# Kernel optimization log

Hardware: AMD Instinct MI355X
Metric: run time of the kernel (lower is better)

The kernel has to match this reference:

```python
import jax, jax.numpy as jnp
import numpy as np

N_NODES = 100000


def _sage_conv(x, src, dst, Wl, Wr, b):
    # mean aggregation of source features onto destination nodes (PyG SAGEConv default)
    msgs = x[src]                                             # [E, d] irregular gather
    agg = jax.ops.segment_sum(msgs, dst, num_segments=N_NODES)
    cnt = jax.ops.segment_sum(jnp.ones((src.shape[0], 1), x.dtype), dst,
                              num_segments=N_NODES)
    agg = agg / jnp.maximum(cnt, 1.0)                         # mean; isolated nodes -> 0
    return agg @ Wl.T + x @ Wr.T + b                          # W_l * agg + W_r * x + b


def setup_inputs() -> dict:
    key = jax.random.key(0)
    ks = jax.random.split(key, 7)
    d_in, d_hid, d_out = 64, 64, 40
    n_edges = 1200000
    x = jax.random.normal(ks[0], (N_NODES, d_in), dtype=jnp.float32)
    edge_index = jax.random.randint(ks[1], (2, n_edges), 0, N_NODES, dtype=jnp.int64)
    s1 = 1.0 / np.sqrt(d_in)
    s2 = 1.0 / np.sqrt(d_hid)
    return {
        "x": x,
        "edge_index": edge_index,
        "W1l": jax.random.normal(ks[2], (d_hid, d_in), dtype=jnp.float32) * s1,
        "W1r": jax.random.normal(ks[3], (d_hid, d_in), dtype=jnp.float32) * s1,
        "b1": jnp.zeros((d_hid,), dtype=jnp.float32),
        "W2l": jax.random.normal(ks[4], (d_out, d_hid), dtype=jnp.float32) * s2,
        "W2r": jax.random.normal(ks[5], (d_out, d_hid), dtype=jnp.float32) * s2,
        "b2": jnp.zeros((d_out,), dtype=jnp.float32),
    }


def reference(x, edge_index, W1l, W1r, b1, W2l, W2r, b2):
    src, dst = edge_index[0], edge_index[1]
    h = _sage_conv(x, src, dst, W1l, W1r, b1)
    h = jax.nn.relu(h)
    # F.dropout(p=0.5) in eval mode is identity (deterministic reference)
    out = _sage_conv(h, src, dst, W2l, W2r, b2)
    return out
```

## Files before the change

kernel.cpp:

```cpp
#include <hip/hip_runtime.h>
#include <hip/hip_bf16.h>

__device__ __forceinline__ float bf2f(unsigned short u) {
    return __uint_as_float(((unsigned int)u) << 16);
}
__device__ __forceinline__ unsigned short f2bf(float f) {
    unsigned int u = __float_as_uint(f);
    return (unsigned short)((u + 0x7FFFu + ((u >> 16) & 1u)) >> 16);
}

__device__ __forceinline__ bool is_i64(const int* __restrict__ e) {
    int z = 0;
#pragma unroll
    for (int i = 0; i < 16; ++i) z |= e[2 * i + 1];
    return z == 0;
}

template <int OUT_DIM, int GST>
__global__ __launch_bounds__(256) void gemm1_hist_fused(
        const float* __restrict__ in, const float* __restrict__ Wl,
        const float* __restrict__ Wr, const float* __restrict__ bias,
        unsigned short* __restrict__ gout, float* __restrict__ sout,
        int n_nodes, int gemmBlocks,
        const int* __restrict__ eidx, int n_edges,
        int* __restrict__ deg, int* __restrict__ rank) {
    __shared__ unsigned int sWp[64][65];
    __shared__ float sB[OUT_DIM];
    __shared__ float sX[4][8][68];

    if ((int)blockIdx.x >= gemmBlocks) {
        const int half = (n_edges + 1) / 2;
        const int e = (blockIdx.x - gemmBlocks) * blockDim.x + threadIdx.x;
        if (e >= half) return;
        const bool i64 = is_i64(eidx);
        {
            int d = i64 ? eidx[2 * (n_edges + e)] : eidx[n_edges + e];
            rank[e] = atomicAdd(&deg[d], 1);
        }
        const int e2 = e + half;
        if (e2 < n_edges) {
            int d = i64 ? eidx[2 * (n_edges + e2)] : eidx[n_edges + e2];
            rank[e2] = atomicAdd(&deg[d], 1);
        }
        return;
    }

    for (int idx = threadIdx.x; idx < OUT_DIM * 64; idx += 256) {
        const int r = idx >> 6, c = idx & 63;
        sWp[c][r] = (unsigned int)f2bf(Wl[idx]) | ((unsigned int)f2bf(Wr[idx]) << 16);
    }
    if (threadIdx.x < OUT_DIM) sB[threadIdx.x] = bias[threadIdx.x];
    __syncthreads();

    const int g = threadIdx.x >> 6;
    const int j = threadIdx.x & 63;
    const bool jv = (j < OUT_DIM);
    const int jj = jv ? j : 0;
    const int blockBase = blockIdx.x * 128;

#pragma unroll 1
    for (int it = 0; it < 4; ++it) {
        const int nb = blockBase + it * 32 + g * 8;
        if (nb >= n_nodes) break;
#pragma unroll
        for (int n = 0; n < 8; ++n) {
            const int node = nb + n;
            sX[g][n][j] = (node < n_nodes) ? in[(size_t)node * 64 + j] : 0.0f;
        }
        float al[8], ar[8];
#pragma unroll
        for (int n = 0; n < 8; ++n) { al[n] = 0.0f; ar[n] = 0.0f; }

#pragma unroll 2
        for (int q = 0; q < 16; ++q) {
            const unsigned int w0 = sWp[4 * q + 0][jj];
            const unsigned int w1 = sWp[4 * q + 1][jj];
            const unsigned int w2 = sWp[4 * q + 2][jj];
            const unsigned int w3 = sWp[4 * q + 3][jj];
            const float4 x0 = *(const float4*)&sX[g][0][4 * q];
            const float4 x1 = *(const float4*)&sX[g][1][4 * q];
            const float4 x2 = *(const float4*)&sX[g][2][4 * q];
            const float4 x3 = *(const float4*)&sX[g][3][4 * q];
            const float4 x4 = *(const float4*)&sX[g][4][4 * q];
            const float4 x5 = *(const float4*)&sX[g][5][4 * q];
            const float4 x6 = *(const float4*)&sX[g][6][4 * q];
            const float4 x7 = *(const float4*)&sX[g][7][4 * q];
#define DG_STEP(WP, M)                                                         \
            {                                                                  \
                const float wl_ = __uint_as_float((WP) << 16);                 \
                const float wr_ = __uint_as_float((WP) & 0xFFFF0000u);         \
                al[0] = fmaf(x0.M, wl_, al[0]); ar[0] = fmaf(x0.M, wr_, ar[0]);\
                al[1] = fmaf(x1.M, wl_, al[1]); ar[1] = fmaf(x1.M, wr_, ar[1]);\
                al[2] = fmaf(x2.M, wl_, al[2]); ar[2] = fmaf(x2.M, wr_, ar[2]);\
                al[3] = fmaf(x3.M, wl_, al[3]); ar[3] = fmaf(x3.M, wr_, ar[3]);\
                al[4] = fmaf(x4.M, wl_, al[4]); ar[4] = fmaf(x4.M, wr_, ar[4]);\
                al[5] = fmaf(x5.M, wl_, al[5]); ar[5] = fmaf(x5.M, wr_, ar[5]);\
                al[6] = fmaf(x6.M, wl_, al[6]); ar[6] = fmaf(x6.M, wr_, ar[6]);\
                al[7] = fmaf(x7.M, wl_, al[7]); ar[7] = fmaf(x7.M, wr_, ar[7]);\
            }
            DG_STEP(w0, x)
            DG_STEP(w1, y)
            DG_STEP(w2, z)
            DG_STEP(w3, w)
#undef DG_STEP
        }

        const float bb = jv ? sB[jj] : 0.0f;
#pragma unroll
        for (int n = 0; n < 8; ++n) {
            const int node = nb + n;
            if (node < n_nodes) {
                if (jv) {
                    gout[(size_t)node * GST + j] = f2bf(al[n]);
                    sout[(size_t)node * OUT_DIM + j] = ar[n] + bb;
                } else if (j < GST) {
                    gout[(size_t)node * GST + j] = 0;
                }
            }
        }
    }
}

__global__ void hist_rank_kernel(const int* __restrict__ eidx, int n_edges,
                                 int* __restrict__ deg, int* __restrict__ rank) {
    const int half = (n_edges + 1) / 2;
    const int e = blockIdx.x * blockDim.x + threadIdx.x;
    if (e >= half) return;
    const bool i64 = is_i64(eidx);
    {
        int d = i64 ? eidx[2 * (n_edges + e)] : eidx[n_edges + e];
        rank[e] = atomicAdd(&deg[d], 1);
    }
    const int e2 = e + half;
    if (e2 < n_edges) {
        int d = i64 ? eidx[2 * (n_edges + e2)] : eidx[n_edges + e2];
        rank[e2] = atomicAdd(&deg[d], 1);
    }
}

__global__ void fill_rank_kernel(const int* __restrict__ eidx, int n_edges,
                                 const int* __restrict__ off, const int* __restrict__ rank,
                                 int* __restrict__ csr) {
    const int half = (n_edges + 1) / 2;
    const int e = blockIdx.x * blockDim.x + threadIdx.x;
    if (e >= half) return;
    const bool i64 = is_i64(eidx);
    {
        int s, d;
        if (i64) { s = eidx[2 * e]; d = eidx[2 * (n_edges + e)]; }
        else     { s = eidx[e];     d = eidx[n_edges + e]; }
        __builtin_nontemporal_store(s, &csr[off[d] + rank[e]]);
    }
    const int e2 = e + half;
    if (e2 < n_edges) {
        int s, d;
        if (i64) { s = eidx[2 * e2]; d = eidx[2 * (n_edges + e2)]; }
        else     { s = eidx[e2];     d = eidx[n_edges + e2]; }
        __builtin_nontemporal_store(s, &csr[off[d] + rank[e2]]);
    }
}

__global__ void fill_kernel(const int* __restrict__ eidx, int n_edges,
                            int* __restrict__ cursor, int* __restrict__ csr) {
    int e = blockIdx.x * blockDim.x + threadIdx.x;
    if (e >= n_edges) return;
    const bool i64 = is_i64(eidx);
    int s, d;
    if (i64) { s = eidx[2 * e]; d = eidx[2 * (n_edges + e)]; }
    else     { s = eidx[e];     d = eidx[n_edges + e]; }
    int pos = atomicAdd(&cursor[d], 1);
    csr[pos] = s;
}

#define TILE 1024
__global__ void scan_p1(const int* __restrict__ deg, int* __restrict__ bsum, int n) {
    __shared__ int red[256];
    const int t = threadIdx.x;
    const int base = blockIdx.x * TILE + t * 4;
    int s = 0;
#pragma unroll
    for (int k = 0; k < 4; ++k) { int i = base + k; if (i < n) s += deg[i]; }
    red[t] = s;
    __syncthreads();
    for (int d = 128; d > 0; d >>= 1) {
        if (t < d) red[t] += red[t + d];
        __syncthreads();
    }
    if (t == 0) bsum[blockIdx.x] = red[0];
}

__global__ void scan_p2(int* __restrict__ bsum, int* __restrict__ off, int nb, int n) {
    __shared__ int s[1024];
    const int t = threadIdx.x;
    s[t] = (t < nb) ? bsum[t] : 0;
    __syncthreads();
    for (int d = 1; d < 1024; d <<= 1) {
        int v = (t >= d) ? s[t - d] : 0;
        __syncthreads();
        s[t] += v;
        __syncthreads();
    }
    if (t < nb) bsum[t] = (t == 0) ? 0 : s[t - 1];
    if (t == 0) off[n] = s[nb - 1];
}

__global__ void scan_p3(const int* __restrict__ deg, const int* __restrict__ bsum,
                        int* __restrict__ off, int* __restrict__ cursor, int n) {
    __shared__ int red[256];
    const int t = threadIdx.x;
    const int base = blockIdx.x * TILE + t * 4;
    int v0 = 0, v1 = 0, v2 = 0, v3 = 0;
    if (base + 0 < n) v0 = deg[base + 0];
    if (base + 1 < n) v1 = deg[base + 1];
    if (base + 2 < n) v2 = deg[base + 2];
    if (base + 3 < n) v3 = deg[base + 3];
    const int mysum = v0 + v1 + v2 + v3;
    red[t] = mysum;
    __syncthreads();
    for (int d = 1; d < 256; d <<= 1) {
        int u = (t >= d) ? red[t - d] : 0;
        __syncthreads();
        red[t] += u;
        __syncthreads();
    }
    int run = bsum[blockIdx.x] + red[t] - mysum;
    if (base + 0 < n) { off[base + 0] = run; cursor[base + 0] = run; run += v0; }
    if (base + 1 < n) { off[base + 1] = run; cursor[base + 1] = run; run += v1; }
    if (base + 2 < n) { off[base + 2] = run; cursor[base + 2] = run; run += v2; }
    if (base + 3 < n) { off[base + 3] = run; cursor[base + 3] = run; run += v3; }
}

template <int OUT_DIM, int GST>
__global__ __launch_bounds__(256) void dual_gemm3(
        const float* __restrict__ in,
        const float* __restrict__ Wl, const float* __restrict__ Wr,
        const float* __restrict__ bias,
        unsigned short* __restrict__ gout,
        float* __restrict__ sout,
        int n_nodes) {
    __shared__ unsigned int sWp[64][65];
    __shared__ float sB[OUT_DIM];
    __shared__ float sX[4][8][68];

    for (int idx = threadIdx.x; idx < OUT_DIM * 64; idx += 256) {
        const int r = idx >> 6, c = idx & 63;
        sWp[c][r] = (unsigned int)f2bf(Wl[idx]) | ((unsigned int)f2bf(Wr[idx]) << 16);
    }
    if (threadIdx.x < OUT_DIM) sB[threadIdx.x] = bias[threadIdx.x];
    __syncthreads();

    const int g = threadIdx.x >> 6;
    const int j = threadIdx.x & 63;
    const bool jv = (j < OUT_DIM);
    const int jj = jv ? j : 0;
    const int blockBase = blockIdx.x * 128;

#pragma unroll 1
    for (int it = 0; it < 4; ++it) {
        const int nb = blockBase + it * 32 + g * 8;
        if (nb >= n_nodes) break;
#pragma unroll
        for (int n = 0; n < 8; ++n) {
            const int node = nb + n;
            sX[g][n][j] = (node < n_nodes) ? in[(size_t)node * 64 + j] : 0.0f;
        }
        float al[8], ar[8];
#pragma unroll
        for (int n = 0; n < 8; ++n) { al[n] = 0.0f; ar[n] = 0.0f; }

#pragma unroll 2
        for (int q = 0; q < 16; ++q) {
            const unsigned int w0 = sWp[4 * q + 0][jj];
            const unsigned int w1 = sWp[4 * q + 1][jj];
            const unsigned int w2 = sWp[4 * q + 2][jj];
            const unsigned int w3 = sWp[4 * q + 3][jj];
            const float4 x0 = *(const float4*)&sX[g][0][4 * q];
            const float4 x1 = *(const float4*)&sX[g][1][4 * q];
            const float4 x2 = *(const float4*)&sX[g][2][4 * q];
            const float4 x3 = *(const float4*)&sX[g][3][4 * q];
            const float4 x4 = *(const float4*)&sX[g][4][4 * q];
            const float4 x5 = *(const float4*)&sX[g][5][4 * q];
            const float4 x6 = *(const float4*)&sX[g][6][4 * q];
            const float4 x7 = *(const float4*)&sX[g][7][4 * q];
#define DG_STEP(WP, M)                                                         \
            {                                                                  \
                const float wl_ = __uint_as_float((WP) << 16);                 \
                const float wr_ = __uint_as_float((WP) & 0xFFFF0000u);         \
                al[0] = fmaf(x0.M, wl_, al[0]); ar[0] = fmaf(x0.M, wr_, ar[0]);\
                al[1] = fmaf(x1.M, wl_, al[1]); ar[1] = fmaf(x1.M, wr_, ar[1]);\
                al[2] = fmaf(x2.M, wl_, al[2]); ar[2] = fmaf(x2.M, wr_, ar[2]);\
                al[3] = fmaf(x3.M, wl_, al[3]); ar[3] = fmaf(x3.M, wr_, ar[3]);\
                al[4] = fmaf(x4.M, wl_, al[4]); ar[4] = fmaf(x4.M, wr_, ar[4]);\
                al[5] = fmaf(x5.M, wl_, al[5]); ar[5] = fmaf(x5.M, wr_, ar[5]);\
                al[6] = fmaf(x6.M, wl_, al[6]); ar[6] = fmaf(x6.M, wr_, ar[6]);\
                al[7] = fmaf(x7.M, wl_, al[7]); ar[7] = fmaf(x7.M, wr_, ar[7]);\
            }
            DG_STEP(w0, x)
            DG_STEP(w1, y)
            DG_STEP(w2, z)
            DG_STEP(w3, w)
#undef DG_STEP
        }

        const float bb = jv ? sB[jj] : 0.0f;
#pragma unroll
        for (int n = 0; n < 8; ++n) {
            const int node = nb + n;
            if (node < n_nodes) {
                if (jv) {
                    gout[(size_t)node * GST + j] = f2bf(al[n]);
                    sout[(size_t)node * OUT_DIM + j] = ar[n] + bb;
                } else if (j < GST) {
                    gout[(size_t)node * GST + j] = 0;
                }
            }
        }
    }
}

template <int SRC_STRIDE, int CGROUPS, int OUT_DIM, bool RELU>
__global__ __launch_bounds__(256) void gather_addmul_bf16(
        const unsigned short* __restrict__ gsrc,
        const float* __restrict__ sadd,
        const int* __restrict__ off, const int* __restrict__ csr,
        float* __restrict__ out, int n_nodes) {
    const int l = threadIdx.x & 63;
    const int wave = (int)((blockIdx.x * blockDim.x + threadIdx.x) >> 6);
    const int c = l & 15, r = l >> 4;
    const bool cact = (c < CGROUPS);
    const int n0 = wave * 8;

    for (int n = n0; n < n0 + 8; ++n) {
        if (n >= n_nodes) return;
        const int e0 = off[n], e1 = off[n + 1];
        float4 a0 = {0.f,0.f,0.f,0.f}, a1 = a0, a2 = a0, a3 = a0;
        for (int i = e0; i < e1; i += 16) {
            const int i0 = i + r, i1 = i0 + 4, i2 = i0 + 8, i3 = i0 + 12;
            if (cact && i0 < e1) {
                const int s = csr[i0];
                const ushort4 u = *(const ushort4*)(gsrc + (size_t)s * SRC_STRIDE + 4 * c);
                a0.x += bf2f(u.x); a0.y += bf2f(u.y); a0.z += bf2f(u.z); a0.w += bf2f(u.w);
            }
            if (cact && i1 < e1) {
                const int s = csr[i1];
                const ushort4 u = *(const ushort4*)(gsrc + (size_t)s * SRC_STRIDE + 4 * c);
                a1.x += bf2f(u.x); a1.y += bf2f(u.y); a1.z += bf2f(u.z); a1.w += bf2f(u.w);
            }
            if (cact && i2 < e1) {
                const int s = csr[i2];
                const ushort4 u = *(const ushort4*)(gsrc + (size_t)s * SRC_STRIDE + 4 * c);
                a2.x += bf2f(u.x); a2.y += bf2f(u.y); a2.z += bf2f(u.z); a2.w += bf2f(u.w);
            }
            if (cact && i3 < e1) {
                const int s = csr[i3];
                const ushort4 u = *(const ushort4*)(gsrc + (size_t)s * SRC_STRIDE + 4 * c);
                a3.x += bf2f(u.x); a3.y += bf2f(u.y); a3.z += bf2f(u.z); a3.w += bf2f(u.w);
            }
        }
        float4 a;
        a.x = (a0.x + a1.x) + (a2.x + a3.x);
        a.y = (a0.y + a1.y) + (a2.y + a3.y);
        a.z = (a0.z + a1.z) + (a2.z + a3.z);
        a.w = (a0.w + a1.w) + (a2.w + a3.w);
        a.x += __shfl_xor(a.x, 16); a.y += __shfl_xor(a.y, 16);
        a.z += __shfl_xor(a.z, 16); a.w += __shfl_xor(a.w, 16);
        a.x += __shfl_xor(a.x, 32); a.y += __shfl_xor(a.y, 32);
        a.z += __shfl_xor(a.z, 32); a.w += __shfl_xor(a.w, 32);
        const int deg = e1 - e0;
        const float inv = (deg > 0) ? 1.0f / (float)deg : 0.0f;
        if (4 * l < OUT_DIM) {
            const float4 sv = *(const float4*)(sadd + (size_t)n * OUT_DIM + 4 * l);
            float4 o;
            o.x = fmaf(a.x, inv, sv.x);
            o.y = fmaf(a.y, inv, sv.y);
            o.z = fmaf(a.z, inv, sv.z);
            o.w = fmaf(a.w, inv, sv.w);
            if (RELU) {
                o.x = fmaxf(o.x, 0.f); o.y = fmaxf(o.y, 0.f);
                o.z = fmaxf(o.z, 0.f); o.w = fmaxf(o.w, 0.f);
            }
            *(float4*)(out + (size_t)n * OUT_DIM + 4 * l) = o;
        }
    }
}

#define NPB 32
template <int OUT_DIM, bool RELU>
__global__ __launch_bounds__(512, 8) void fused_layer_f4(
        const float* __restrict__ feat,
        const int* __restrict__ off, const int* __restrict__ csr,
        const float* __restrict__ Wl, const float* __restrict__ Wr,
        const float* __restrict__ bias,
        float* __restrict__ out, int n_nodes) {
    __shared__ float sWl[OUT_DIM][65];
    __shared__ float sWr[OUT_DIM][65];
    __shared__ float sB[OUT_DIM];
    __shared__ float sA[8][64];
    __shared__ float sX[8][64];

    for (int idx = threadIdx.x; idx < OUT_DIM * 64; idx += 512) {
        sWl[idx >> 6][idx & 63] = Wl[idx];
        sWr[idx >> 6][idx & 63] = Wr[idx];
    }
    if (threadIdx.x < OUT_DIM) sB[threadIdx.x] = bias[threadIdx.x];
    __syncthreads();

    const int g = threadIdx.x >> 6;
    const int l = threadIdx.x & 63;
    const int c = l & 15, r = l >> 4;
    const int base = blockIdx.x * NPB;

#pragma unroll 1
    for (int it = 0; it < NPB / 8; ++it) {
        const int node = base + it * 8 + g;
        if (node >= n_nodes) break;
        const int e0 = off[node], e1 = off[node + 1];
        const float selfv = feat[(size_t)node * 64 + l];
        float4 a0 = {0.f,0.f,0.f,0.f}, a1 = a0, a2 = a0, a3 = a0;
        for (int i = e0; i < e1; i += 16) {
            const int i0 = i + r, i1 = i0 + 4, i2 = i0 + 8, i3 = i0 + 12;
            if (i0 < e1) { const int s = csr[i0];
                const float4 v = *(const float4*)(feat + (size_t)s * 64 + 4 * c);
                a0.x += v.x; a0.y += v.y; a0.z += v.z; a0.w += v.w; }
            if (i1 < e1) { const int s = csr[i1];
                const float4 v = *(const float4*)(feat + (size_t)s * 64 + 4 * c);
                a1.x += v.x; a1.y += v.y; a1.z += v.z; a1.w += v.w; }
            if (i2 < e1) { const int s = csr[i2];
                const float4 v = *(const float4*)(feat + (size_t)s * 64 + 4 * c);
                a2.x += v.x; a2.y += v.y; a2.z += v.z; a2.w += v.w; }
            if (i3 < e1) { const int s = csr[i3];
                const float4 v = *(const float4*)(feat + (size_t)s * 64 + 4 * c);
                a3.x += v.x; a3.y += v.y; a3.z += v.z; a3.w += v.w; }
        }
        float4 a;
        a.x = (a0.x + a1.x) + (a2.x + a3.x);
        a.y = (a0.y + a1.y) + (a2.y + a3.y);
        a.z = (a0.z + a1.z) + (a2.z + a3.z);
        a.w = (a0.w + a1.w) + (a2.w + a3.w);
        a.x += __shfl_xor(a.x, 16); a.y += __shfl_xor(a.y, 16);
        a.z += __shfl_xor(a.z, 16); a.w += __shfl_xor(a.w, 16);
        a.x += __shfl_xor(a.x, 32); a.y += __shfl_xor(a.y, 32);
        a.z += __shfl_xor(a.z, 32); a.w += __shfl_xor(a.w, 32);
        const int deg = e1 - e0;
        const float inv = (deg > 0) ? 1.0f / (float)deg : 0.0f;
        if (l < 16) {
            float4 s4;
            s4.x = a.x * inv; s4.y = a.y * inv; s4.z = a.z * inv; s4.w = a.w * inv;
            *(float4*)&sA[g][4 * l] = s4;
        }
        sX[g][l] = selfv;
        if (l < OUT_DIM) {
            float acc = sB[l];
#pragma unroll
            for (int k = 0; k < 64; ++k) {
                acc = fmaf(sA[g][k], sWl[l][k], acc);
                acc = fmaf(sX[g][k], sWr[l][k], acc);
            }
            if (RELU) acc = fmaxf(acc, 0.0f);
            out[(size_t)node * OUT_DIM + l] = acc;
        }
    }
}

template <int OUT_DIM, bool RELU, bool FEAT_BF16, bool OUT_BF16>
__global__ __launch_bounds__(512, 8) void fused_layer(
        const void* __restrict__ feat,
        const int* __restrict__ off, const int* __restrict__ csr,
        const float* __restrict__ Wl, const float* __restrict__ Wr,
        const float* __restrict__ bias,
        void* __restrict__ out, int n_nodes) {
    __shared__ float sWl[OUT_DIM][65];
    __shared__ float sWr[OUT_DIM][65];
    __shared__ float sB[OUT_DIM];
    __shared__ float sA[8][64];
    __shared__ float sX[8][64];

    for (int idx = threadIdx.x; idx < OUT_DIM * 64; idx += 512) {
        sWl[idx >> 6][idx & 63] = Wl[idx];
        sWr[idx >> 6][idx & 63] = Wr[idx];
    }
    if (threadIdx.x < OUT_DIM) sB[threadIdx.x] = bias[threadIdx.x];
    __syncthreads();

    const int g = threadIdx.x >> 6;
    const int j = threadIdx.x & 63;
    const int base = blockIdx.x * NPB;

#pragma unroll 1
    for (int it = 0; it < NPB / 8; ++it) {
        const int node = base + it * 8 + g;
        if (node >= n_nodes) break;
        const int e0 = off[node], e1 = off[node + 1];
        float a0 = 0.f, a1 = 0.f, a2 = 0.f, a3 = 0.f;
        int i = e0;
        while (i < e1) {
            const int cnt = ((e1 - i) < 64) ? (e1 - i) : 64;
            const int eid = (j < cnt) ? csr[i + j] : 0;
            int t = 0;
            for (; t + 3 < cnt; t += 4) {
                const int s0 = __shfl(eid, t);
                const int s1 = __shfl(eid, t + 1);
                const int s2 = __shfl(eid, t + 2);
                const int s3 = __shfl(eid, t + 3);
                if (FEAT_BF16) {
                    a0 += bf2f(((const unsigned short*)feat)[(size_t)s0 * 64 + j]);
                    a1 += bf2f(((const unsigned short*)feat)[(size_t)s1 * 64 + j]);
                    a2 += bf2f(((const unsigned short*)feat)[(size_t)s2 * 64 + j]);
                    a3 += bf2f(((const unsigned short*)feat)[(size_t)s3 * 64 + j]);
                } else {
                    a0 += ((const float*)feat)[(size_t)s0 * 64 + j];
                    a1 += ((const float*)feat)[(size_t)s1 * 64 + j];
                    a2 += ((const float*)feat)[(size_t)s2 * 64 + j];
                    a3 += ((const float*)feat)[(size_t)s3 * 64 + j];
                }
            }
            for (; t < cnt; ++t) {
                const int s0 = __shfl(eid, t);
                a0 += FEAT_BF16 ? bf2f(((const unsigned short*)feat)[(size_t)s0 * 64 + j])
                                : ((const float*)feat)[(size_t)s0 * 64 + j];
            }
            i += cnt;
        }
        const int deg = e1 - e0;
        const float inv = (deg > 0) ? 1.0f / (float)deg : 0.0f;
        sA[g][j] = ((a0 + a1) + (a2 + a3)) * inv;
        sX[g][j] = FEAT_BF16 ? bf2f(((const unsigned short*)feat)[(size_t)node * 64 + j])
                             : ((const float*)feat)[(size_t)node * 64 + j];
        if (j < OUT_DIM) {
            float acc = sB[j];
#pragma unroll
            for (int k = 0; k < 64; ++k) {
                acc = fmaf(sA[g][k], sWl[j][k], acc);
                acc = fmaf(sX[g][k], sWr[j][k], acc);
            }
            if (RELU) acc = fmaxf(acc, 0.0f);
            if (OUT_BF16)
                ((unsigned short*)out)[(size_t)node * OUT_DIM + j] = f2bf(acc);
            else
                ((float*)out)[(size_t)node * OUT_DIM + j] = acc;
        }
    }
}

extern "C" void kernel_launch(void* const* d_in, const int* in_sizes, int n_in,
                              void* d_out, int out_size, void* d_ws, size_t ws_size,
                              hipStream_t stream) {
    const float* x   = (const float*)d_in[0];
    const int*   ei  = (const int*)d_in[1];
    const float* W1l = (const float*)d_in[2];
    const float* W1r = (const float*)d_in[3];
    const float* b1  = (const float*)d_in[4];
    const float* W2l = (const float*)d_in[5];
    const float* W2r = (const float*)d_in[6];
    const float* b2  = (const float*)d_in[7];
    float* out = (float*)d_out;

    const int n_nodes = in_sizes[0] / 64;
    const int n_edges = in_sizes[1] / 2;

    const size_t off_b  = (size_t)(n_nodes + 1) * sizeof(int);
    const size_t cur_b  = (size_t)n_nodes * sizeof(int);
    const size_t csr_b  = (size_t)n_edges * sizeof(int);
    const size_t rank_b = (size_t)n_edges * sizeof(int);
    const size_t bsum_b = 1024 * sizeof(int);
    const size_t g1_b   = (size_t)n_nodes * 64 * sizeof(unsigned short);
    const size_t s1_b   = (size_t)n_nodes * 64 * sizeof(float);
    const size_t g2_b   = (size_t)n_nodes * 48 * sizeof(unsigned short);
    const size_t h_b    = (size_t)n_nodes * 64 * sizeof(float);
    const size_t reg1_b = g1_b + s1_b;

    char* p = (char*)d_ws;
    int* off    = (int*)p;  p += off_b;
    int* cursor = (int*)p;  p += cur_b;
    int* csr    = (int*)p;  p += csr_b;
    int* rank   = (int*)p;  p += rank_b;
    int* bsum   = (int*)p;  p += bsum_b;
    size_t used = ((size_t)(p - (char*)d_ws) + 255) / 256 * 256;
    p = (char*)d_ws + used;

    const bool tierA = ws_size >= used + reg1_b + h_b;
    const bool tierC = ws_size >= used + h_b;

    unsigned short* g1 = (unsigned short*)p;
    float*          s1 = (float*)(p + g1_b);
    float*          h  = (float*)(p + reg1_b);
    unsigned short* g2 = (unsigned short*)p;
    float*          s2 = (float*)(p + g2_b);

    hipMemsetAsync(cursor, 0, cur_b, stream);

    const int half = (n_edges + 1) / 2;
    const int hblocks = (half + 255) / 256;
    const int gemmBlocks   = (n_nodes + 127) / 128;
    const int gatherBlocks = (n_nodes + 31) / 32;
    const int fusedBlocks  = (n_nodes + NPB - 1) / NPB;
    const int nb = (n_nodes + TILE - 1) / TILE;
    const int eblocks = (n_edges + 255) / 256;

    if (tierA) {
        gemm1_hist_fused<64, 64><<<gemmBlocks + hblocks, 256, 0, stream>>>(
            x, W1l, W1r, b1, g1, s1, n_nodes, gemmBlocks,
            ei, n_edges, cursor, rank);
        scan_p1<<<nb, 256, 0, stream>>>(cursor, bsum, n_nodes);
        scan_p2<<<1, 1024, 0, stream>>>(bsum, off, nb, n_nodes);
        scan_p3<<<nb, 256, 0, stream>>>(cursor, bsum, off, cursor, n_nodes);
        fill_rank_kernel<<<hblocks, 256, 0, stream>>>(ei, n_edges, off, rank, csr);

        gather_addmul_bf16<64, 16, 64, true><<<gatherBlocks, 256, 0, stream>>>(
            g1, s1, off, csr, h, n_nodes);
        dual_gemm3<40, 48><<<gemmBlocks, 256, 0, stream>>>(
            h, W2l, W2r, b2, g2, s2, n_nodes);
        gather_addmul_bf16<48, 10, 40, false><<<gatherBlocks, 256, 0, stream>>>(
            g2, s2, off, csr, out, n_nodes);
    } else {
        hist_rank_kernel<<<hblocks, 256, 0, stream>>>(ei, n_edges, cursor, rank);
        scan_p1<<<nb, 256, 0, stream>>>(cursor, bsum, n_nodes);
        scan_p2<<<1, 1024, 0, stream>>>(bsum, off, nb, n_nodes);
        scan_p3<<<nb, 256, 0, stream>>>(cursor, bsum, off, cursor, n_nodes);
        fill_kernel<<<eblocks, 256, 0, stream>>>(ei, n_edges, cursor, csr);

        if (tierC) {
            float* hh = (float*)p;
            fused_layer_f4<64, true><<<fusedBlocks, 512, 0, stream>>>(
                x, off, csr, W1l, W1r, b1, hh, n_nodes);
            fused_layer_f4<40, false><<<fusedBlocks, 512, 0, stream>>>(
                hh, off, csr, W2l, W2r, b2, out, n_nodes);
        } else {
            void* hh = (void*)p;
            fused_layer<64, true, false, true><<<fusedBlocks, 512, 0, stream>>>(
                x, off, csr, W1l, W1r, b1, hh, n_nodes);
            fused_layer<40, false, true, false><<<fusedBlocks, 512, 0, stream>>>(
                hh, off, csr, W2l, W2r, b2, out, n_nodes);
        }
    }
}
```

Before: 285.3 us.

## Fuse layer-1 mean gather with layer-2 dual GEMM into one kernel

```diff
diff --git a/kernel.cpp b/kernel.cpp
--- a/kernel.cpp
+++ b/kernel.cpp
@@ -121,118 +121,11 @@
     }
 }
 
-__global__ void hist_rank_kernel(const int* __restrict__ eidx, int n_edges,
-                                 int* __restrict__ deg, int* __restrict__ rank) {
-    const int half = (n_edges + 1) / 2;
-    const int e = blockIdx.x * blockDim.x + threadIdx.x;
-    if (e >= half) return;
-    const bool i64 = is_i64(eidx);
-    {
-        int d = i64 ? eidx[2 * (n_edges + e)] : eidx[n_edges + e];
-        rank[e] = atomicAdd(&deg[d], 1);
-    }
-    const int e2 = e + half;
-    if (e2 < n_edges) {
-        int d = i64 ? eidx[2 * (n_edges + e2)] : eidx[n_edges + e2];
-        rank[e2] = atomicAdd(&deg[d], 1);
-    }
-}
-
-__global__ void fill_rank_kernel(const int* __restrict__ eidx, int n_edges,
-                                 const int* __restrict__ off, const int* __restrict__ rank,
-                                 int* __restrict__ csr) {
-    const int half = (n_edges + 1) / 2;
-    const int e = blockIdx.x * blockDim.x + threadIdx.x;
-    if (e >= half) return;
-    const bool i64 = is_i64(eidx);
-    {
-        int s, d;
-        if (i64) { s = eidx[2 * e]; d = eidx[2 * (n_edges + e)]; }
-        else     { s = eidx[e];     d = eidx[n_edges + e]; }
-        __builtin_nontemporal_store(s, &csr[off[d] + rank[e]]);
-    }
-    const int e2 = e + half;
-    if (e2 < n_edges) {
-        int s, d;
-        if (i64) { s = eidx[2 * e2]; d = eidx[2 * (n_edges + e2)]; }
-        else     { s = eidx[e2];     d = eidx[n_edges + e2]; }
-        __builtin_nontemporal_store(s, &csr[off[d] + rank[e2]]);
-    }
-}
-
-__global__ void fill_kernel(const int* __restrict__ eidx, int n_edges,
-                            int* __restrict__ cursor, int* __restrict__ csr) {
-    int e = blockIdx.x * blockDim.x + threadIdx.x;
-    if (e >= n_edges) return;
-    const bool i64 = is_i64(eidx);
-    int s, d;
-    if (i64) { s = eidx[2 * e]; d = eidx[2 * (n_edges + e)]; }
-    else     { s = eidx[e];     d = eidx[n_edges + e]; }
-    int pos = atomicAdd(&cursor[d], 1);
-    csr[pos] = s;
-}
-
-#define TILE 1024
-__global__ void scan_p1(const int* __restrict__ deg, int* __restrict__ bsum, int n) {
-    __shared__ int red[256];
-    const int t = threadIdx.x;
-    const int base = blockIdx.x * TILE + t * 4;
-    int s = 0;
-#pragma unroll
-    for (int k = 0; k < 4; ++k) { int i = base + k; if (i < n) s += deg[i]; }
-    red[t] = s;
-    __syncthreads();
-    for (int d = 128; d > 0; d >>= 1) {
-        if (t < d) red[t] += red[t + d];
-        __syncthreads();
-    }
-    if (t == 0) bsum[blockIdx.x] = red[0];
-}
-
-__global__ void scan_p2(int* __restrict__ bsum, int* __restrict__ off, int nb, int n) {
-    __shared__ int s[1024];
-    const int t = threadIdx.x;
-    s[t] = (t < nb) ? bsum[t] : 0;
-    __syncthreads();
-    for (int d = 1; d < 1024; d <<= 1) {
-        int v = (t >= d) ? s[t - d] : 0;
-        __syncthreads();
-        s[t] += v;
-        __syncthreads();
-    }
-    if (t < nb) bsum[t] = (t == 0) ? 0 : s[t - 1];
-    if (t == 0) off[n] = s[nb - 1];
-}
-
-__global__ void scan_p3(const int* __restrict__ deg, const int* __restrict__ bsum,
-                        int* __restrict__ off, int* __restrict__ cursor, int n) {
-    __shared__ int red[256];
-    const int t = threadIdx.x;
-    const int base = blockIdx.x * TILE + t * 4;
-    int v0 = 0, v1 = 0, v2 = 0, v3 = 0;
-    if (base + 0 < n) v0 = deg[base + 0];
-    if (base + 1 < n) v1 = deg[base + 1];
-    if (base + 2 < n) v2 = deg[base + 2];
-    if (base + 3 < n) v3 = deg[base + 3];
-    const int mysum = v0 + v1 + v2 + v3;
-    red[t] = mysum;
-    __syncthreads();
-    for (int d = 1; d < 256; d <<= 1) {
-        int u = (t >= d) ? red[t - d] : 0;
-        __syncthreads();
-        red[t] += u;
-        __syncthreads();
-    }
-    int run = bsum[blockIdx.x] + red[t] - mysum;
-    if (base + 0 < n) { off[base + 0] = run; cursor[base + 0] = run; run += v0; }
-    if (base + 1 < n) { off[base + 1] = run; cursor[base + 1] = run; run += v1; }
-    if (base + 2 < n) { off[base + 2] = run; cursor[base + 2] = run; run += v2; }
-    if (base + 3 < n) { off[base + 3] = run; cursor[base + 3] = run; run += v3; }
-}
-
 template <int OUT_DIM, int GST>
-__global__ __launch_bounds__(256) void dual_gemm3(
-        const float* __restrict__ in,
+__global__ __launch_bounds__(256) void gather_gemm_fused(
+        const unsigned short* __restrict__ gsrc,
+        const float* __restrict__ sadd,
+        const int* __restrict__ off, const int* __restrict__ csr,
         const float* __restrict__ Wl, const float* __restrict__ Wr,
         const float* __restrict__ bias,
         unsigned short* __restrict__ gout,
@@ -251,19 +144,73 @@
 
     const int g = threadIdx.x >> 6;
     const int j = threadIdx.x & 63;
+    const int c = j & 15, r4 = j >> 4;
     const bool jv = (j < OUT_DIM);
     const int jj = jv ? j : 0;
-    const int blockBase = blockIdx.x * 128;
+    const int blockBase = blockIdx.x * 64;
 
 #pragma unroll 1
-    for (int it = 0; it < 4; ++it) {
+    for (int it = 0; it < 2; ++it) {
         const int nb = blockBase + it * 32 + g * 8;
         if (nb >= n_nodes) break;
-#pragma unroll
+
+#pragma unroll 1
         for (int n = 0; n < 8; ++n) {
             const int node = nb + n;
-            sX[g][n][j] = (node < n_nodes) ? in[(size_t)node * 64 + j] : 0.0f;
-        }
+            if (node >= n_nodes) {
+                if (j < 16) {
+                    float4 z = {0.f, 0.f, 0.f, 0.f};
+                    *(float4*)&sX[g][n][4 * j] = z;
+                }
+                continue;
+            }
+            const int e0 = off[node], e1 = off[node + 1];
+            float4 a0 = {0.f,0.f,0.f,0.f}, a1 = a0, a2 = a0, a3 = a0;
+            for (int i = e0; i < e1; i += 16) {
+                const int i0 = i + r4, i1 = i0 + 4, i2 = i0 + 8, i3 = i0 + 12;
+                if (i0 < e1) {
+                    const int s = csr[i0];
+                    const ushort4 u = *(const ushort4*)(gsrc + (size_t)s * 64 + 4 * c);
+                    a0.x += bf2f(u.x); a0.y += bf2f(u.y); a0.z += bf2f(u.z); a0.w += bf2f(u.w);
+                }
+                if (i1 < e1) {
+                    const int s = csr[i1];
+                    const ushort4 u = *(const ushort4*)(gsrc + (size_t)s * 64 + 4 * c);
+                    a1.x += bf2f(u.x); a1.y += bf2f(u.y); a1.z += bf2f(u.z); a1.w += bf2f(u.w);
+                }
+                if (i2 < e1) {
+                    const int s = csr[i2];
+                    const ushort4 u = *(const ushort4*)(gsrc + (size_t)s * 64 + 4 * c);
+                    a2.x += bf2f(u.x); a2.y += bf2f(u.y); a2.z += bf2f(u.z); a2.w += bf2f(u.w);
+                }
+                if (i3 < e1) {
+                    const int s = csr[i3];
+                    const ushort4 u = *(const ushort4*)(gsrc + (size_t)s * 64 + 4 * c);
+                    a3.x += bf2f(u.x); a3.y += bf2f(u.y); a3.z += bf2f(u.z); a3.w += bf2f(u.w);
+                }
+            }
+            float4 a;
+            a.x = (a0.x + a1.x) + (a2.x + a3.x);
+            a.y = (a0.y + a1.y) + (a2.y + a3.y);
+            a.z = (a0.z + a1.z) + (a2.z + a3.z);
+            a.w = (a0.w + a1.w) + (a2.w + a3.w);
+            a.x += __shfl_xor(a.x, 16); a.y += __shfl_xor(a.y, 16);
+            a.z += __shfl_xor(a.z, 16); a.w += __shfl_xor(a.w, 16);
+            a.x += __shfl_xor(a.x, 32); a.y += __shfl_xor(a.y, 32);
+            a.z += __shfl_xor(a.z, 32); a.w += __shfl_xor(a.w, 32);
+            const int deg = e1 - e0;
+            const float inv = (deg > 0) ? 1.0f / (float)deg : 0.0f;
+            if (j < 16) {
+                const float4 sv = *(const float4*)(sadd + (size_t)node * 64 + 4 * j);
+                float4 o;
+                o.x = fmaxf(fmaf(a.x, inv, sv.x), 0.f);
+                o.y = fmaxf(fmaf(a.y, inv, sv.y), 0.f);
+                o.z = fmaxf(fmaf(a.z, inv, sv.z), 0.f);
+                o.w = fmaxf(fmaf(a.w, inv, sv.w), 0.f);
+                *(float4*)&sX[g][n][4 * j] = o;
+            }
+        }
+
         float al[8], ar[8];
 #pragma unroll
         for (int n = 0; n < 8; ++n) { al[n] = 0.0f; ar[n] = 0.0f; }
@@ -318,6 +265,115 @@
     }
 }
 
+__global__ void hist_rank_kernel(const int* __restrict__ eidx, int n_edges,
+                                 int* __restrict__ deg, int* __restrict__ rank) {
+    const int half = (n_edges + 1) / 2;
+    const int e = blockIdx.x * blockDim.x + threadIdx.x;
+    if (e >= half) return;
+    const bool i64 = is_i64(eidx);
+    {
+        int d = i64 ? eidx[2 * (n_edges + e)] : eidx[n_edges + e];
+        rank[e] = atomicAdd(&deg[d], 1);
+    }
+    const int e2 = e + half;
+    if (e2 < n_edges) {
+        int d = i64 ? eidx[2 * (n_edges + e2)] : eidx[n_edges + e2];
+        rank[e2] = atomicAdd(&deg[d], 1);
+    }
+}
+
+__global__ void fill_rank_kernel(const int* __restrict__ eidx, int n_edges,
+                                 const int* __restrict__ off, const int* __restrict__ rank,
+                                 int* __restrict__ csr) {
+    const int half = (n_edges + 1) / 2;
+    const int e = blockIdx.x * blockDim.x + threadIdx.x;
+    if (e >= half) return;
+    const bool i64 = is_i64(eidx);
+    {
+        int s, d;
+        if (i64) { s = eidx[2 * e]; d = eidx[2 * (n_edges + e)]; }
+        else     { s = eidx[e];     d = eidx[n_edges + e]; }
+        __builtin_nontemporal_store(s, &csr[off[d] + rank[e]]);
+    }
+    const int e2 = e + half;
+    if (e2 < n_edges) {
+        int s, d;
+        if (i64) { s = eidx[2 * e2]; d = eidx[2 * (n_edges + e2)]; }
+        else     { s = eidx[e2];     d = eidx[n_edges + e2]; }
+        __builtin_nontemporal_store(s, &csr[off[d] + rank[e2]]);
+    }
+}
+
+__global__ void fill_kernel(const int* __restrict__ eidx, int n_edges,
+                            int* __restrict__ cursor, int* __restrict__ csr) {
+    int e = blockIdx.x * blockDim.x + threadIdx.x;
+    if (e >= n_edges) return;
+    const bool i64 = is_i64(eidx);
+    int s, d;
+    if (i64) { s = eidx[2 * e]; d = eidx[2 * (n_edges + e)]; }
+    else     { s = eidx[e];     d = eidx[n_edges + e]; }
+    int pos = atomicAdd(&cursor[d], 1);
+    csr[pos] = s;
+}
+
+#define TILE 1024
+__global__ void scan_p1(const int* __restrict__ deg, int* __restrict__ bsum, int n) {
+    __shared__ int red[256];
+    const int t = threadIdx.x;
+    const int base = blockIdx.x * TILE + t * 4;
+    int s = 0;
+#pragma unroll
+    for (int k = 0; k < 4; ++k) { int i = base + k; if (i < n) s += deg[i]; }
+    red[t] = s;
+    __syncthreads();
+    for (int d = 128; d > 0; d >>= 1) {
+        if (t < d) red[t] += red[t + d];
+        __syncthreads();
+    }
+    if (t == 0) bsum[blockIdx.x] = red[0];
+}
+
+__global__ void scan_p2(int* __restrict__ bsum, int* __restrict__ off, int nb, int n) {
+    __shared__ int s[1024];
+    const int t = threadIdx.x;
+    s[t] = (t < nb) ? bsum[t] : 0;
+    __syncthreads();
+    for (int d = 1; d < 1024; d <<= 1) {
+        int v = (t >= d) ? s[t - d] : 0;
+        __syncthreads();
+        s[t] += v;
+        __syncthreads();
+    }
+    if (t < nb) bsum[t] = (t == 0) ? 0 : s[t - 1];
+    if (t == 0) off[n] = s[nb - 1];
+}
+
+__global__ void scan_p3(const int* __restrict__ deg, const int* __restrict__ bsum,
+                        int* __restrict__ off, int* __restrict__ cursor, int n) {
+    __shared__ int red[256];
+    const int t = threadIdx.x;
+    const int base = blockIdx.x * TILE + t * 4;
+    int v0 = 0, v1 = 0, v2 = 0, v3 = 0;
+    if (base + 0 < n) v0 = deg[base + 0];
+    if (base + 1 < n) v1 = deg[base + 1];
+    if (base + 2 < n) v2 = deg[base + 2];
+    if (base + 3 < n) v3 = deg[base + 3];
+    const int mysum = v0 + v1 + v2 + v3;
+    red[t] = mysum;
+    __syncthreads();
+    for (int d = 1; d < 256; d <<= 1) {
+        int u = (t >= d) ? red[t - d] : 0;
+        __syncthreads();
+        red[t] += u;
+        __syncthreads();
+    }
+    int run = bsum[blockIdx.x] + red[t] - mysum;
+    if (base + 0 < n) { off[base + 0] = run; cursor[base + 0] = run; run += v0; }
+    if (base + 1 < n) { off[base + 1] = run; cursor[base + 1] = run; run += v1; }
+    if (base + 2 < n) { off[base + 2] = run; cursor[base + 2] = run; run += v2; }
+    if (base + 3 < n) { off[base + 3] = run; cursor[base + 3] = run; run += v3; }
+}
+
 template <int SRC_STRIDE, int CGROUPS, int OUT_DIM, bool RELU>
 __global__ __launch_bounds__(256) void gather_addmul_bf16(
         const unsigned short* __restrict__ gsrc,
@@ -578,14 +634,14 @@
     size_t used = ((size_t)(p - (char*)d_ws) + 255) / 256 * 256;
     p = (char*)d_ws + used;
 
-    const bool tierA = ws_size >= used + reg1_b + h_b;
+    const size_t s2_b = (size_t)n_nodes * 40 * sizeof(float);
+    const bool tierA = ws_size >= used + reg1_b + g2_b + s2_b;
     const bool tierC = ws_size >= used + h_b;
 
     unsigned short* g1 = (unsigned short*)p;
     float*          s1 = (float*)(p + g1_b);
-    float*          h  = (float*)(p + reg1_b);
-    unsigned short* g2 = (unsigned short*)p;
-    float*          s2 = (float*)(p + g2_b);
+    unsigned short* g2 = (unsigned short*)(p + reg1_b);
+    float*          s2 = (float*)(p + reg1_b + g2_b);
 
     hipMemsetAsync(cursor, 0, cur_b, stream);
 
@@ -593,6 +649,7 @@
     const int hblocks = (half + 255) / 256;
     const int gemmBlocks   = (n_nodes + 127) / 128;
     const int gatherBlocks = (n_nodes + 31) / 32;
+    const int ggBlocks     = (n_nodes + 63) / 64;
     const int fusedBlocks  = (n_nodes + NPB - 1) / NPB;
     const int nb = (n_nodes + TILE - 1) / TILE;
     const int eblocks = (n_edges + 255) / 256;
@@ -606,10 +663,8 @@
         scan_p3<<<nb, 256, 0, stream>>>(cursor, bsum, off, cursor, n_nodes);
         fill_rank_kernel<<<hblocks, 256, 0, stream>>>(ei, n_edges, off, rank, csr);
 
-        gather_addmul_bf16<64, 16, 64, true><<<gatherBlocks, 256, 0, stream>>>(
-            g1, s1, off, csr, h, n_nodes);
-        dual_gemm3<40, 48><<<gemmBlocks, 256, 0, stream>>>(
-            h, W2l, W2r, b2, g2, s2, n_nodes);
+        gather_gemm_fused<40, 48><<<ggBlocks, 256, 0, stream>>>(
+            g1, s1, off, csr, W2l, W2r, b2, g2, s2, n_nodes);
         gather_addmul_bf16<48, 10, 40, false><<<gatherBlocks, 256, 0, stream>>>(
             g2, s2, off, csr, out, n_nodes);
     } else {
```

New measurement: 301.0 us. 1.05x slower.
